# Performance work log

Hardware: AMD Instinct MI355X
Metric: run time of the kernel (lower is better)

Reference implementation:

```python
import jax, jax.numpy as jnp
import numpy as np

TEMPERATURE = 0.2

def setup_inputs() -> dict:
    key = jax.random.key(0)
    k1, k2 = jax.random.split(key)
    B, D = 4096, 128
    emb_i = jax.random.normal(k1, (B, D), dtype=jnp.float32)
    emb_j = jax.random.normal(k2, (B, D), dtype=jnp.float32)
    return {"emb_i": emb_i, "emb_j": emb_j}

def reference(emb_i, emb_j):
    # L2-normalize each embedding row, concat -> z: [2B, D]
    z_i = emb_i / jnp.linalg.norm(emb_i, axis=1, keepdims=True)
    z_j = emb_j / jnp.linalg.norm(emb_j, axis=1, keepdims=True)
    z = jnp.concatenate([z_i, z_j], axis=0)          # [2B, D]
    N2 = z.shape[0]
    N = N2 // 2
    # cosine similarity of normalized vectors == dot product
    sim = z @ z.T                                    # [2B, 2B]
    logits = sim / TEMPERATURE
    # denominator excludes only the diagonal (k != i)
    diag_mask = jnp.eye(N2, dtype=bool)
    masked = jnp.where(diag_mask, -jnp.inf, logits)
    lse = jax.nn.logsumexp(masked, axis=1)           # [2B]
    # positive pair for row i is i+N (mod 2N)
    pos_idx = jnp.concatenate([jnp.arange(N) + N, jnp.arange(N)])
    pos_logits = jnp.take_along_axis(logits, pos_idx[:, None], axis=1)[:, 0]
    # loss = (1/2N) * sum_i -log( exp(pos_i) / sum_{k!=i} exp(logits[i,k]) )
    loss = jnp.mean(lse - pos_logits)
    return loss
```

## Files before the change

kernel.cpp:

```cpp
#include <hip/hip_runtime.h>
#include <hip/hip_bf16.h>

typedef __attribute__((ext_vector_type(8))) short bf16x8;
typedef __attribute__((ext_vector_type(4))) float f32x4;

#define EXP_SCALE 7.213475204444817f

__device__ __forceinline__ float fast_exp2(float x) {
#if __has_builtin(__builtin_amdgcn_exp2f)
  return __builtin_amdgcn_exp2f(x);
#else
  return exp2f(x);
#endif
}

__device__ __forceinline__ unsigned short f32_to_bf16(float f) {
  unsigned int u = __float_as_uint(f);
  unsigned int r = (u + 0x7FFFu + ((u >> 16) & 1u)) >> 16;
  return (unsigned short)r;
}


__global__ __launch_bounds__(256) void k_normalize(
    const float* __restrict__ emb_i, const float* __restrict__ emb_j,
    unsigned short* __restrict__ z, float* __restrict__ rowsum,
    float* __restrict__ out)
{
  if (blockIdx.x == 0 && threadIdx.x == 0) out[0] = 0.0f;
  if (threadIdx.x < 4) rowsum[(blockIdx.x << 2) + threadIdx.x] = 0.0f;
  const int w = threadIdx.x >> 6;
  const int lane = threadIdx.x & 63;
  const int row = (blockIdx.x << 2) + w;
  const float* src = (row < 4096) ? (emb_i + row * 128) : (emb_j + (row - 4096) * 128);
  float2 v = reinterpret_cast<const float2*>(src)[lane];
  float ss = v.x * v.x + v.y * v.y;
  #pragma unroll
  for (int m = 1; m < 64; m <<= 1) ss += __shfl_xor(ss, m, 64);
  float rinv = 1.0f / sqrtf(ss);
  ushort2 st;
  st.x = f32_to_bf16(v.x * rinv);
  st.y = f32_to_bf16(v.y * rinv);
  const int e = lane << 1;
  const int kk = e >> 5;
  const int q = (e >> 3) & 3;
  const int rem = e & 7;
  const int tile = row >> 4;
  const int c = row & 15;
  unsigned short* dst = z + tile * 2048 + kk * 512 + ((q << 4) + c) * 8 + rem;
  *reinterpret_cast<ushort2*>(dst) = st;
}

__global__ __launch_bounds__(256, 3) void k_simlse(
    const unsigned short* __restrict__ z,
    float* __restrict__ rowsum,
    float* __restrict__ rowpos)
{
  const int w = threadIdx.x >> 6;
  const int lane = threadIdx.x & 63;
  const int q = lane >> 4;
  const int c = lane & 15;

  int ch = 0;
  while ((int)blockIdx.x >= 4 * (ch + 1) * (ch + 2)) ++ch;
  const int rb = blockIdx.x - 4 * ch * (ch + 1);
  const int R0 = rb << 6;
  const bool upper = (rb < (ch << 3));

  __shared__ short smem[8192];
  {
    const unsigned short* zA = z + (R0 >> 4) * 2048;
    #pragma unroll
    for (int j = 0; j < 4; ++j) {
      const int v = (j << 8) + threadIdx.x;
      *reinterpret_cast<bf16x8*>(&smem[v << 3]) =
          *reinterpret_cast<const bf16x8*>(zA + (v << 3));
    }
  }
  __syncthreads();
  bf16x8 a[4][4];
  #pragma unroll
  for (int rg = 0; rg < 4; ++rg)
    #pragma unroll
    for (int kk = 0; kk < 4; ++kk)
      a[rg][kk] = *reinterpret_cast<const bf16x8*>(
          &smem[rg * 2048 + kk * 512 + (lane << 3)]);

  float acc[4][4];
  #pragma unroll
  for (int rg = 0; rg < 4; ++rg)
    #pragma unroll
    for (int e = 0; e < 4; ++e) acc[rg][e] = 0.0f;
  float pacc[4] = {0.f, 0.f, 0.f, 0.f};

  __shared__ float colacc[512];
  __shared__ float lsum[4][64];
  __shared__ float lpos[4][16];

  const int ct0 = (ch << 5) + w;
  const unsigned short* bwave = z + ct0 * 2048 + (lane << 3);

  const int pos0t = ((R0 + 4096) & 8191) >> 4;
  const int ipb = ((pos0t >> 5) == ch) ? ((pos0t & 31) >> 2) : -99;

  bf16x8 b0[4], b1[4];
  auto ldb = [&](bf16x8 (&dst)[4], int idx) {
    const unsigned short* p = bwave + idx * 8192;
    dst[0] = *reinterpret_cast<const bf16x8*>(p);
    dst[1] = *reinterpret_cast<const bf16x8*>(p + 512);
    dst[2] = *reinterpret_cast<const bf16x8*>(p + 1024);
    dst[3] = *reinterpret_cast<const bf16x8*>(p + 1536);
  };

  auto process = [&](const bf16x8 (&bb)[4], int i) {
    f32x4 cc[4];
    #pragma unroll
    for (int rr = 0; rr < 4; ++rr) cc[rr] = f32x4{0.f, 0.f, 0.f, 0.f};
    #pragma unroll
    for (int kk = 0; kk < 4; ++kk)
      #pragma unroll
      for (int rr = 0; rr < 4; ++rr)
        cc[rr] = __builtin_amdgcn_mfma_f32_16x16x32_bf16(
            a[rr][kk], bb[kk], cc[rr], 0, 0, 0);
    float colp0 = 0.0f, colp1 = 0.0f;
    #pragma unroll
    for (int rr = 0; rr < 4; ++rr)
      #pragma unroll
      for (int e = 0; e < 4; ++e) {
        float t = fast_exp2(__builtin_fmaf(cc[rr][e], EXP_SCALE, -EXP_SCALE));
        acc[rr][e] += t;
        if (upper) { if (rr & 1) colp1 += t; else colp0 += t; }
      }
    if (upper) {
      float colp = colp0 + colp1;
      colp += __shfl_xor(colp, 16, 64);
      colp += __shfl_xor(colp, 32, 64);
      if (lane < 16)
        colacc[(((i << 2) + w) << 4) + c] = colp;
    }
    if (i == ipb) {
      #pragma unroll
      for (int rr = 0; rr < 4; ++rr) {
        if (rr == w) {
          #pragma unroll
          for (int e = 0; e < 4; ++e)
            if (c == ((q << 2) + e)) pacc[e] = cc[rr][e] * 5.0f;
        }
      }
    }
  };

  ldb(b0, 0);
  #pragma unroll 1
  for (int i = 0; i < 8; i += 2) {
    ldb(b1, i + 1);
    process(b0, i);
    if (i + 2 < 8) ldb(b0, i + 2);
    process(b1, i + 1);
  }

  #pragma unroll
  for (int m = 1; m < 16; m <<= 1) {
    #pragma unroll
    for (int rg = 0; rg < 4; ++rg)
      #pragma unroll
      for (int e = 0; e < 4; ++e)
        acc[rg][e] += __shfl_xor(acc[rg][e], m, 64);
    #pragma unroll
    for (int e = 0; e < 4; ++e) pacc[e] += __shfl_xor(pacc[e], m, 64);
  }

  if (c == 0) {
    #pragma unroll
    for (int rg = 0; rg < 4; ++rg)
      #pragma unroll
      for (int e = 0; e < 4; ++e)
        lsum[w][rg * 16 + (q << 2) + e] = acc[rg][e];
    #pragma unroll
    for (int e = 0; e < 4; ++e) lpos[w][(q << 2) + e] = pacc[e];
  }
  __syncthreads();

  if (threadIdx.x < 64) {
    const int t = threadIdx.x;
    float s = lsum[0][t] + lsum[1][t] + lsum[2][t] + lsum[3][t];
    atomicAdd(&rowsum[R0 + t], s);
    if (ipb != -99)
      rowpos[R0 + t] = lpos[t >> 4][t & 15];
  }
  if (upper) {
    #pragma unroll
    for (int j = 0; j < 2; ++j) {
      const int idx = (j << 8) + threadIdx.x;
      atomicAdd(&rowsum[(ch << 9) + idx], colacc[idx]);
    }
  }
}

__global__ __launch_bounds__(256) void k_finish(
    const float* __restrict__ rowsum, const float* __restrict__ rowpos,
    float* __restrict__ out)
{
  const int r = blockIdx.x * 256 + threadIdx.x;
  float tot = rowsum[r] - 1.0f;
  float v = 5.0f + logf(tot) - rowpos[r & 4095];
  #pragma unroll
  for (int m = 1; m < 64; m <<= 1) v += __shfl_xor(v, m, 64);
  __shared__ float red[4];
  if ((threadIdx.x & 63) == 0) red[threadIdx.x >> 6] = v;
  __syncthreads();
  if (threadIdx.x == 0)
    atomicAdd(out, (red[0] + red[1] + red[2] + red[3]) * (1.0f / 8192.0f));
}

extern "C" void kernel_launch(void* const* d_in, const int* in_sizes, int n_in,
                              void* d_out, int out_size, void* d_ws, size_t ws_size,
                              hipStream_t stream) {
  const float* emb_i = (const float*)d_in[0];
  const float* emb_j = (const float*)d_in[1];
  unsigned short* z = (unsigned short*)d_ws;
  float* rowsum = (float*)((char*)d_ws + 8192 * 128 * 2);
  float* rowpos = rowsum + 8192;
  float* out = (float*)d_out;

  k_normalize<<<2048, 256, 0, stream>>>(emb_i, emb_j, z, rowsum, out);
  k_simlse<<<1088, 256, 0, stream>>>(z, rowsum, rowpos);
  k_finish<<<32, 256, 0, stream>>>(rowsum, rowpos, out);
}
```

Before: 78.95 us.

## Replace global atomic row/column sum accumulation with partial buffers reduced in finish

Row and column exp-sums from each similarity block are no longer accumulated with global atomicAdd. Instead they are written to per-chunk and per-row-block partial buffers (rpart, cpart), and k_finish sums the relevant partials for each row. This removes atomic contention and the shared colacc staging, along with the need to zero rowsum in the normalize kernel. In exchange, k_finish reads up to about 140 strided partials per row with only 32 blocks, and workspace use grows to several MB.

```diff
diff --git a/kernel.cpp b/kernel.cpp
--- a/kernel.cpp
+++ b/kernel.cpp
@@ -23,11 +23,9 @@
 
 __global__ __launch_bounds__(256) void k_normalize(
     const float* __restrict__ emb_i, const float* __restrict__ emb_j,
-    unsigned short* __restrict__ z, float* __restrict__ rowsum,
-    float* __restrict__ out)
+    unsigned short* __restrict__ z, float* __restrict__ out)
 {
   if (blockIdx.x == 0 && threadIdx.x == 0) out[0] = 0.0f;
-  if (threadIdx.x < 4) rowsum[(blockIdx.x << 2) + threadIdx.x] = 0.0f;
   const int w = threadIdx.x >> 6;
   const int lane = threadIdx.x & 63;
   const int row = (blockIdx.x << 2) + w;
@@ -52,7 +50,8 @@
 
 __global__ __launch_bounds__(256, 3) void k_simlse(
     const unsigned short* __restrict__ z,
-    float* __restrict__ rowsum,
+    float* __restrict__ rpart,
+    float* __restrict__ cpart,
     float* __restrict__ rowpos)
 {
   const int w = threadIdx.x >> 6;
@@ -92,7 +91,6 @@
     for (int e = 0; e < 4; ++e) acc[rg][e] = 0.0f;
   float pacc[4] = {0.f, 0.f, 0.f, 0.f};
 
-  __shared__ float colacc[512];
   __shared__ float lsum[4][64];
   __shared__ float lpos[4][16];
 
@@ -135,7 +133,7 @@
       colp += __shfl_xor(colp, 16, 64);
       colp += __shfl_xor(colp, 32, 64);
       if (lane < 16)
-        colacc[(((i << 2) + w) << 4) + c] = colp;
+        cpart[(rb << 13) + (((ct0 + (i << 2)) << 4) + c)] = colp;
     }
     if (i == ipb) {
       #pragma unroll
@@ -183,25 +181,27 @@
   if (threadIdx.x < 64) {
     const int t = threadIdx.x;
     float s = lsum[0][t] + lsum[1][t] + lsum[2][t] + lsum[3][t];
-    atomicAdd(&rowsum[R0 + t], s);
+    rpart[(ch << 13) + R0 + t] = s;
     if (ipb != -99)
       rowpos[R0 + t] = lpos[t >> 4][t & 15];
   }
-  if (upper) {
-    #pragma unroll
-    for (int j = 0; j < 2; ++j) {
-      const int idx = (j << 8) + threadIdx.x;
-      atomicAdd(&rowsum[(ch << 9) + idx], colacc[idx]);
-    }
-  }
 }
 
 __global__ __launch_bounds__(256) void k_finish(
-    const float* __restrict__ rowsum, const float* __restrict__ rowpos,
-    float* __restrict__ out)
+    const float* __restrict__ rpart, const float* __restrict__ cpart,
+    const float* __restrict__ rowpos, float* __restrict__ out)
 {
   const int r = blockIdx.x * 256 + threadIdx.x;
-  float tot = rowsum[r] - 1.0f;
+  const int chr = r >> 9;
+  float t0 = -1.0f, t1 = 0.0f;
+  for (int ch = chr; ch < 16; ++ch) t0 += rpart[(ch << 13) + r];
+  const int nrb = chr << 3;
+  #pragma unroll 4
+  for (int rb = 0; rb < nrb; rb += 2) {
+    t0 += cpart[(rb << 13) + r];
+    t1 += cpart[((rb + 1) << 13) + r];
+  }
+  float tot = t0 + t1;
   float v = 5.0f + logf(tot) - rowpos[r & 4095];
   #pragma unroll
   for (int m = 1; m < 64; m <<= 1) v += __shfl_xor(v, m, 64);
@@ -218,11 +218,12 @@
   const float* emb_i = (const float*)d_in[0];
   const float* emb_j = (const float*)d_in[1];
   unsigned short* z = (unsigned short*)d_ws;
-  float* rowsum = (float*)((char*)d_ws + 8192 * 128 * 2);
-  float* rowpos = rowsum + 8192;
+  float* rpart = (float*)((char*)d_ws + (2 << 20));
+  float* cpart = rpart + 16 * 8192;
+  float* rowpos = cpart + 128 * 8192;
   float* out = (float*)d_out;
 
-  k_normalize<<<2048, 256, 0, stream>>>(emb_i, emb_j, z, rowsum, out);
-  k_simlse<<<1088, 256, 0, stream>>>(z, rowsum, rowpos);
-  k_finish<<<32, 256, 0, stream>>>(rowsum, rowpos, out);
-}
+  k_normalize<<<2048, 256, 0, stream>>>(emb_i, emb_j, z, out);
+  k_simlse<<<1088, 256, 0, stream>>>(z, rpart, cpart, rowpos);
+  k_finish<<<32, 256, 0, stream>>>(rpart, cpart, rowpos, out);
+}
```

After: 83.11 us. 1.05x slower.
